# Kernel tuning notes

Measured on AMD Instinct MI355X. Metric: run time of the kernel, lower is better.

The kernel has to match this reference:

```python
import jax, jax.numpy as jnp
import numpy as np

N, E, B, EP = 100000, 1600000, 512, 200000
NIN, NEMB, HID, NL = 64, 64, 72, 3
EPS = 1e-5


def setup_inputs() -> dict:
    key = jax.random.key(0)
    ks = jax.random.split(key, 20)
    inp = {
        'x': jax.random.normal(ks[0], (N, NIN), jnp.float32),
        'emb': jax.random.normal(ks[1], (N, NEMB), jnp.float32),
        'assign': jax.random.uniform(ks[2], (N, B), jnp.float32),
        'edge_index': jax.random.randint(ks[3], (2, E), 0, N, jnp.int64),
        'pedge_index': jax.random.randint(ks[4], (2, EP), 0, B, jnp.int64),
        # params (xavier-ish scale)
        'node_w': jax.random.normal(ks[5], (NIN, HID), jnp.float32) / np.sqrt(NIN),
        'node_b': jnp.zeros((HID,), jnp.float32),
        'emb_w': jax.random.normal(ks[6], (NEMB, HID), jnp.float32) / np.sqrt(NEMB),
        'emb_b': jnp.zeros((HID,), jnp.float32),
        'conv_winit': jax.random.normal(ks[7], (NL, HID, HID), jnp.float32) / np.sqrt(HID),
        'conv_wroot': jax.random.normal(ks[8], (NL, HID, HID), jnp.float32) / np.sqrt(HID),
        'conv_bias': jnp.zeros((NL, HID), jnp.float32),
        'bn_gamma': jnp.ones((NL, HID), jnp.float32),
        'bn_beta': jnp.zeros((NL, HID), jnp.float32),
        'mlp_w1': jax.random.normal(ks[9], (12 * HID, HID), jnp.float32) / np.sqrt(12 * HID),
        'mlp_b1': jnp.zeros((HID,), jnp.float32),
        'mlp_w2': jax.random.normal(ks[10], (HID, 1), jnp.float32) / np.sqrt(HID),
        'mlp_b2': jnp.zeros((1,), jnp.float32),
    }
    return inp


def _forward(x, emb, assign, node_w, node_b, emb_w, emb_b, conv_winit,
             conv_wroot, conv_bias, bn_gamma, bn_beta, mlp_w1, mlp_b1,
             mlp_w2, mlp_b2, edge_index, pedge_index):
    n = x.shape[0]
    nb = assign.shape[1]
    row, col = edge_index[0], edge_index[1]
    # gcn_norm without self-loops (ARMAConv): D^{-1/2} A D^{-1/2}
    deg = jax.ops.segment_sum(jnp.ones((row.shape[0],), x.dtype), col, num_segments=n)
    dis = jnp.where(deg > 0, jax.lax.rsqrt(jnp.maximum(deg, 1.0)) * jnp.where(deg > 0, 1.0, 0.0), 0.0)
    dis = jnp.where(deg > 0, deg ** -0.5, 0.0)
    norm = dis[row] * dis[col]

    h = jax.nn.relu(x @ node_w + node_b)  # [N, HID]
    for l in range(NL):
        # ARMAConv K=1, T=1: relu(A_hat (h Wi) + h Wr + b)
        m = norm[:, None] * (h @ conv_winit[l])[row]        # [E, HID]
        agg = jax.ops.segment_sum(m, col, num_segments=n)   # [N, HID]
        h = jax.nn.relu(agg + h @ conv_wroot[l] + conv_bias[l])
        # F.relu applied again in forward (idempotent), then BatchNorm (training stats)
        mu = h.mean(0)
        var = ((h - mu) ** 2).mean(0)
        h = (h - mu) * jax.lax.rsqrt(var + EPS) * bn_gamma[l] + bn_beta[l]

    e = jax.nn.relu(emb @ emb_w + emb_b)
    z = jnp.concatenate([h, e], axis=-1)  # [N, 2*HID]

    batch = jnp.argmax(assign, axis=-1)
    cnt = jax.ops.segment_sum(jnp.ones((n,), z.dtype), batch, num_segments=nb)
    p1 = jax.ops.segment_sum(z, batch, num_segments=nb)
    p2 = jax.ops.segment_max(z, batch, num_segments=nb)
    p3 = p1 / jnp.maximum(cnt, 1.0)[:, None]
    xp = jnp.concatenate([p1, p2, p3], axis=-1)  # [B, 6*HID]

    pair = jnp.concatenate([xp[pedge_index[0]], xp[pedge_index[1]]], axis=1)  # [EP, 12*HID]
    out = jnp.tanh(pair @ mlp_w1 + mlp_b1) @ mlp_w2 + mlp_b2
    return out


def reference(x, emb, assign, edge_index, pedge_index, node_w, node_b, emb_w,
              emb_b, conv_winit, conv_wroot, conv_bias, bn_gamma, bn_beta,
              mlp_w1, mlp_b1, mlp_w2, mlp_b2):
    return _forward(x, emb, assign, node_w, node_b, emb_w, emb_b, conv_winit,
                    conv_wroot, conv_bias, bn_gamma, bn_beta, mlp_w1, mlp_b1,
                    mlp_w2, mlp_b2, edge_index, pedge_index)
```

## Files before the change

kernel.cpp:

```cpp
#include <hip/hip_runtime.h>
#include <hip/hip_bf16.h>

#define HID 72
#define EPSV 1e-5f
#define CAP 64

__device__ __forceinline__ float tanh_fast(float x) {
    float cx = fminf(fmaxf(x, -15.f), 15.f);
    float e = __expf(2.f * cx);
    return __fdividef(e - 1.f, e + 1.f);
}
__device__ __forceinline__ void fma4(float4& a, float w, const float4 v) {
    a.x += w * v.x; a.y += w * v.y; a.z += w * v.z; a.w += w * v.w;
}

__global__ void k_init(int* deg, float* stats, int* bcnt, int N, int statlen, int B) {
    int i = blockIdx.x * blockDim.x + threadIdx.x;
    if (i < N) deg[i] = 0;
    if (i < statlen) stats[i] = 0.f;
    if (i < B) bcnt[i] = 0;
}

__global__ __launch_bounds__(256) void k_fillcap(const int* __restrict__ row, const int* __restrict__ col,
                                                 int* __restrict__ deg, int* __restrict__ csr_r, int E) {
    int e = blockIdx.x * blockDim.x + threadIdx.x;
    if (e < E) {
        int c = col[e];
        int pos = atomicAdd(&deg[c], 1);
        if (pos < CAP) csr_r[(size_t)c * CAP + pos] = row[e];
    }
}

__global__ void k_dis(const int* __restrict__ deg, float* __restrict__ dis, int N) {
    int i = blockIdx.x * blockDim.x + threadIdx.x;
    if (i < N) {
        int d = deg[i];
        dis[i] = (d > 0) ? rsqrtf((float)d) : 0.f;
    }
}

#define DP 76
template <int K>
__global__ __launch_bounds__(256) void k_dense_t(const float* __restrict__ xin, const float* __restrict__ W,
                                                 const float* __restrict__ bias, float* __restrict__ out, int N) {
    __shared__ float hs[128][DP];
    __shared__ float ws[HID][DP];
    int tid = threadIdx.x;
    int n0 = blockIdx.x * 128;
    for (int i = tid; i < K * HID; i += 256) {
        int k = i / HID, f = i % HID;
        ws[f][k] = W[i];
    }
    for (int i = tid; i < 128 * K; i += 256) {
        int n = i / K, f = i % K;
        int gn = n0 + n;
        hs[n][f] = (gn < N) ? xin[(size_t)gn * K + f] : 0.f;
    }
    __syncthreads();
    int tn = tid & 31;
    int tf = (tid >> 5) * 9;
    float acc[4][9];
    #pragma unroll
    for (int j = 0; j < 9; j++) {
        float b = bias[tf + j];
        acc[0][j] = b; acc[1][j] = b; acc[2][j] = b; acc[3][j] = b;
    }
    #pragma unroll 2
    for (int k4 = 0; k4 < K / 4; k4++) {
        int k = k4 * 4;
        float4 h0 = *(const float4*)&hs[tn][k];
        float4 h1 = *(const float4*)&hs[tn + 32][k];
        float4 h2 = *(const float4*)&hs[tn + 64][k];
        float4 h3 = *(const float4*)&hs[tn + 96][k];
        #pragma unroll
        for (int j = 0; j < 9; j++) {
            float4 w = *(const float4*)&ws[tf + j][k];
            acc[0][j] += h0.x * w.x + h0.y * w.y + h0.z * w.z + h0.w * w.w;
            acc[1][j] += h1.x * w.x + h1.y * w.y + h1.z * w.z + h1.w * w.w;
            acc[2][j] += h2.x * w.x + h2.y * w.y + h2.z * w.z + h2.w * w.w;
            acc[3][j] += h3.x * w.x + h3.y * w.y + h3.z * w.z + h3.w * w.w;
        }
    }
    #pragma unroll
    for (int i = 0; i < 4; i++) {
        int gn = n0 + tn + 32 * i;
        if (gn >= N) continue;
        float* dst = out + (size_t)gn * HID + tf;
        #pragma unroll
        for (int j = 0; j < 9; j++) dst[j] = fmaxf(acc[i][j], 0.f);
    }
}

#define CP 76
template <bool BN>
__global__ __launch_bounds__(256) void k_conv_t(const float* t, const float* __restrict__ stats,
                                                const float* __restrict__ gamma, const float* __restrict__ beta,
                                                const float* __restrict__ wi, const float* __restrict__ wr,
                                                const float* __restrict__ cb, float* __restrict__ hw,
                                                float* agg, int N, float invN) {
    __shared__ float hs[64][CP];
    __shared__ float ws[2 * HID][CP];
    int tid = threadIdx.x;
    int n0 = blockIdx.x * 64;
    for (int i = tid; i < HID * 2 * HID; i += 256) {
        int k = i / (2 * HID), f = i % (2 * HID);
        ws[f][k] = (f < HID) ? wi[k * HID + f] : wr[k * HID + (f - HID)];
    }
    for (int i = tid; i < 64 * HID; i += 256) {
        int n = i / HID, f = i % HID;
        int gn = n0 + n;
        float v = (gn < N) ? t[(size_t)gn * HID + f] : 0.f;
        if constexpr (BN) {
            float mu = stats[f] * invN;
            float var = stats[HID + f] * invN - mu * mu;
            v = (v - mu) * rsqrtf(var + EPSV) * gamma[f] + beta[f];
        }
        hs[n][f] = v;
    }
    __syncthreads();
    int tn = tid & 15;
    int tf = (tid >> 4) * 9;
    float acc[4][9];
    #pragma unroll
    for (int j = 0; j < 9; j++) {
        float b = (tf >= HID) ? cb[tf - HID + j] : 0.f;
        acc[0][j] = b; acc[1][j] = b; acc[2][j] = b; acc[3][j] = b;
    }
    #pragma unroll 2
    for (int k4 = 0; k4 < HID / 4; k4++) {
        int k = k4 * 4;
        float4 h0 = *(const float4*)&hs[tn][k];
        float4 h1 = *(const float4*)&hs[tn + 16][k];
        float4 h2 = *(const float4*)&hs[tn + 32][k];
        float4 h3 = *(const float4*)&hs[tn + 48][k];
        #pragma unroll
        for (int j = 0; j < 9; j++) {
            float4 w = *(const float4*)&ws[tf + j][k];
            acc[0][j] += h0.x * w.x + h0.y * w.y + h0.z * w.z + h0.w * w.w;
            acc[1][j] += h1.x * w.x + h1.y * w.y + h1.z * w.z + h1.w * w.w;
            acc[2][j] += h2.x * w.x + h2.y * w.y + h2.z * w.z + h2.w * w.w;
            acc[3][j] += h3.x * w.x + h3.y * w.y + h3.z * w.z + h3.w * w.w;
        }
    }
    #pragma unroll
    for (int i = 0; i < 4; i++) {
        int gn = n0 + tn + 16 * i;
        if (gn >= N) continue;
        float* dst = (tf < HID) ? (hw + (size_t)gn * HID + tf) : (agg + (size_t)gn * HID + (tf - HID));
        #pragma unroll
        for (int j = 0; j < 9; j++) dst[j] = acc[i][j];
    }
}

__global__ __launch_bounds__(256) void k_gather9(const float* __restrict__ hw, const int* __restrict__ deg,
                                                 const int* __restrict__ csr_r, const float* __restrict__ dis,
                                                 float* t, int N) {
    int tid = blockIdx.x * blockDim.x + threadIdx.x;
    int n = tid / 9;
    int s = tid - n * 9;
    if (n >= N) return;
    float4* trow = (float4*)(t + (size_t)n * HID) + s * 2;
    float4 a0 = trow[0], a1 = trow[1];
    int d = deg[n];
    d = (d > CAP) ? CAP : d;
    float disc = dis[n];
    const int* crow = csr_r + (size_t)n * CAP;
    const float4* hb = (const float4*)hw + s * 2;
    for (int j0 = 0; j0 < d; j0 += 4) {
        int4 rr = *(const int4*)(crow + j0);
        int rem = d - j0;
        {
            float w = disc * dis[rr.x];
            const float4* hp = hb + (size_t)rr.x * 18;
            fma4(a0, w, hp[0]); fma4(a1, w, hp[1]);
        }
        if (rem > 1) {
            float w = disc * dis[rr.y];
            const float4* hp = hb + (size_t)rr.y * 18;
            fma4(a0, w, hp[0]); fma4(a1, w, hp[1]);
        }
        if (rem > 2) {
            float w = disc * dis[rr.z];
            const float4* hp = hb + (size_t)rr.z * 18;
            fma4(a0, w, hp[0]); fma4(a1, w, hp[1]);
        }
        if (rem > 3) {
            float w = disc * dis[rr.w];
            const float4* hp = hb + (size_t)rr.w * 18;
            fma4(a0, w, hp[0]); fma4(a1, w, hp[1]);
        }
    }
    trow[0] = make_float4(fmaxf(a0.x, 0.f), fmaxf(a0.y, 0.f), fmaxf(a0.z, 0.f), fmaxf(a0.w, 0.f));
    trow[1] = make_float4(fmaxf(a1.x, 0.f), fmaxf(a1.y, 0.f), fmaxf(a1.z, 0.f), fmaxf(a1.w, 0.f));
}

__global__ __launch_bounds__(256) void k_stats(const float* __restrict__ t, float* __restrict__ st, int total4) {
    __shared__ float s1[HID], s2[HID];
    int tx = threadIdx.x;
    if (tx < HID) s1[tx] = 0.f;
    else if (tx < 2 * HID) s2[tx - HID] = 0.f;
    __syncthreads();
    int stride = gridDim.x * blockDim.x;
    int i0 = blockIdx.x * blockDim.x + tx;
    int f0 = (i0 * 4) % HID;
    float a0 = 0, a1 = 0, a2 = 0, a3 = 0, q0 = 0, q1 = 0, q2 = 0, q3 = 0;
    const float4* tp = (const float4*)t;
    for (int i = i0; i < total4; i += stride) {
        float4 v = tp[i];
        a0 += v.x; q0 += v.x * v.x;
        a1 += v.y; q1 += v.y * v.y;
        a2 += v.z; q2 += v.z * v.z;
        a3 += v.w; q3 += v.w * v.w;
    }
    atomicAdd(&s1[f0 + 0], a0); atomicAdd(&s2[f0 + 0], q0);
    atomicAdd(&s1[f0 + 1], a1); atomicAdd(&s2[f0 + 1], q1);
    atomicAdd(&s1[f0 + 2], a2); atomicAdd(&s2[f0 + 2], q2);
    atomicAdd(&s1[f0 + 3], a3); atomicAdd(&s2[f0 + 3], q3);
    __syncthreads();
    if (tx < HID) {
        atomicAdd(&st[tx], s1[tx]);
        atomicAdd(&st[HID + tx], s2[tx]);
    }
}

__global__ __launch_bounds__(256) void k_argmax(const float* __restrict__ assign, int* __restrict__ batchv,
                                                int* __restrict__ bcnt, int N, int B) {
    int wib = threadIdx.x >> 6;
    int lane = threadIdx.x & 63;
    int n = blockIdx.x * (blockDim.x >> 6) + wib;
    if (n >= N) return;
    const float4* rp4 = (const float4*)(assign + (size_t)n * B);
    float best = -INFINITY;
    int bidx = 0x7fffffff;
    int nq = B / 4;
    for (int q = lane; q < nq; q += 64) {
        float4 v = rp4[q];
        int j = q * 4;
        if (v.x > best) { best = v.x; bidx = j; }
        if (v.y > best) { best = v.y; bidx = j + 1; }
        if (v.z > best) { best = v.z; bidx = j + 2; }
        if (v.w > best) { best = v.w; bidx = j + 3; }
    }
    #pragma unroll
    for (int off = 32; off > 0; off >>= 1) {
        float ov = __shfl_down(best, off);
        int oi = __shfl_down(bidx, off);
        if (ov > best || (ov == best && oi < bidx)) { best = ov; bidx = oi; }
    }
    if (lane == 0) {
        batchv[n] = bidx;
        atomicAdd(&bcnt[bidx], 1);
    }
}

__global__ __launch_bounds__(1024) void k_bscan(const int* __restrict__ bcnt, int* __restrict__ boffs,
                                                int* __restrict__ bcur, int B) {
    __shared__ int lds[1024];
    int t = threadIdx.x;
    int v = (t < B) ? bcnt[t] : 0;
    lds[t] = v;
    __syncthreads();
    for (int off = 1; off < 1024; off <<= 1) {
        int x = (t >= off) ? lds[t - off] : 0;
        __syncthreads();
        lds[t] += x;
        __syncthreads();
    }
    if (t < B) {
        int excl = lds[t] - v;
        boffs[t] = excl;
        bcur[t] = excl;
    }
}

__global__ void k_bfill(const int* __restrict__ batchv, int* __restrict__ bcur, int* __restrict__ nlist, int N) {
    int n = blockIdx.x * blockDim.x + threadIdx.x;
    if (n < N) {
        int b = batchv[n];
        int pos = atomicAdd(&bcur[b], 1);
        nlist[pos] = n;
    }
}

__global__ __launch_bounds__(576) void k_poolB(const float* __restrict__ t2, const float* __restrict__ ebuf,
                                               const float* __restrict__ stats2, const float* __restrict__ g2,
                                               const float* __restrict__ bt2, const int* __restrict__ boffs,
                                               const int* __restrict__ bcnt, const int* __restrict__ nlist,
                                               float* __restrict__ xp, float invN) {
    __shared__ float ls[4][2 * HID], lm[4][2 * HID];
    int b = blockIdx.x;
    int tid = threadIdx.x;
    int f = tid % (2 * HID);
    int ch = tid / (2 * HID);
    bool isH = f < HID;
    float a = 1.f, sh = 0.f;
    const float* src;
    if (isH) {
        float s1v = stats2[f], s2v = stats2[HID + f];
        float mu = s1v * invN;
        float var = s2v * invN - mu * mu;
        float inv = rsqrtf(var + EPSV);
        a = inv * g2[f];
        sh = bt2[f] - mu * a;
        src = t2 + f;
    } else {
        src = ebuf + (f - HID);
    }
    int s = boffs[b];
    int c = bcnt[b];
    int e = s + c;
    float sum = 0.f, mx = -INFINITY;
    for (int i = s + ch; i < e; i += 4) {
        float v = src[(size_t)nlist[i] * HID] * a + sh;
        sum += v;
        mx = fmaxf(mx, v);
    }
    ls[ch][f] = sum;
    lm[ch][f] = mx;
    __syncthreads();
    if (ch == 0) {
        float stot = ls[0][f] + ls[1][f] + ls[2][f] + ls[3][f];
        float mtot = fmaxf(fmaxf(lm[0][f], lm[1][f]), fmaxf(lm[2][f], lm[3][f]));
        float* xr = xp + (size_t)b * (6 * HID);
        xr[f] = stot;
        xr[2 * HID + f] = mtot;
        xr[4 * HID + f] = stot / fmaxf((float)c, 1.f);
    }
}

__global__ __launch_bounds__(192) void k_uv(const float* __restrict__ xp, const float* __restrict__ w1,
                                            const float* __restrict__ b1, float* __restrict__ U,
                                            float* __restrict__ V) {
    int b = blockIdx.x;
    int t = threadIdx.x;
    if (t >= 2 * HID) return;
    int half = t / HID;
    int f = t % HID;
    const float* xr = xp + (size_t)b * (6 * HID);
    const float* wb = w1 + (size_t)half * (6 * HID) * HID + f;
    float acc = (half == 0) ? b1[f] : 0.f;
    #pragma unroll 4
    for (int k = 0; k < 6 * HID; k++) acc += xr[k] * wb[(size_t)k * HID];
    if (half == 0) U[(size_t)b * HID + f] = acc;
    else           V[(size_t)b * HID + f] = acc;
}

__global__ __launch_bounds__(256) void k_edge(const int* __restrict__ pe, const float* __restrict__ U,
                                              const float* __restrict__ V, const float* __restrict__ w2,
                                              const float* __restrict__ b2, float* __restrict__ out, int EP) {
    int ep = blockIdx.x * blockDim.x + threadIdx.x;
    if (ep >= EP) return;
    int a = pe[ep];
    int b = pe[EP + ep];
    const float4* up = (const float4*)(U + (size_t)a * HID);
    const float4* vp = (const float4*)(V + (size_t)b * HID);
    float s = 0.f;
    #pragma unroll
    for (int q = 0; q < HID / 4; q++) {
        float4 u = up[q];
        float4 v = vp[q];
        s += tanh_fast(u.x + v.x) * w2[q * 4 + 0];
        s += tanh_fast(u.y + v.y) * w2[q * 4 + 1];
        s += tanh_fast(u.z + v.z) * w2[q * 4 + 2];
        s += tanh_fast(u.w + v.w) * w2[q * 4 + 3];
    }
    out[ep] = s + b2[0];
}

extern "C" void kernel_launch(void* const* d_in, const int* in_sizes, int n_in,
                              void* d_out, int out_size, void* d_ws, size_t ws_size,
                              hipStream_t stream) {
    const float* x       = (const float*)d_in[0];
    const float* emb     = (const float*)d_in[1];
    const float* assign  = (const float*)d_in[2];
    const int*   ei      = (const int*)d_in[3];
    const int*   pe      = (const int*)d_in[4];
    const float* node_w  = (const float*)d_in[5];
    const float* node_b  = (const float*)d_in[6];
    const float* emb_w   = (const float*)d_in[7];
    const float* emb_b   = (const float*)d_in[8];
    const float* conv_wi = (const float*)d_in[9];
    const float* conv_wr = (const float*)d_in[10];
    const float* conv_b  = (const float*)d_in[11];
    const float* bn_g    = (const float*)d_in[12];
    const float* bn_b    = (const float*)d_in[13];
    const float* w1      = (const float*)d_in[14];
    const float* b1      = (const float*)d_in[15];
    const float* w2      = (const float*)d_in[16];
    const float* b2      = (const float*)d_in[17];

    int N = in_sizes[0] / 64;
    int B = in_sizes[2] / N;
    int E = in_sizes[3] / 2;
    int EP = in_sizes[4] / 2;
    float invN = 1.0f / (float)N;

    char* wp = (char*)d_ws;
    auto alloc = [&](size_t nbytes) -> void* {
        void* p = (void*)wp;
        wp += (nbytes + 255) & ~(size_t)255;
        return p;
    };
    float* t_buf  = (float*)alloc((size_t)N * HID * 4);
    float* hw     = (float*)alloc((size_t)N * HID * 4);
    float* e_buf  = (float*)alloc((size_t)N * HID * 4);
    int*   csr_r  = (int*)alloc((size_t)N * CAP * 4);
    int*   deg    = (int*)alloc((size_t)N * 4);
    float* dis    = (float*)alloc((size_t)N * 4);
    int*   batchv = (int*)alloc((size_t)N * 4);
    int*   nlist  = (int*)alloc((size_t)N * 4);
    float* stats  = (float*)alloc((size_t)3 * 2 * HID * 4);
    int*   bcnt   = (int*)alloc((size_t)B * 4);
    int*   boffs  = (int*)alloc((size_t)B * 4);
    int*   bcur   = (int*)alloc((size_t)B * 4);
    float* xp     = (float*)alloc((size_t)B * 6 * HID * 4);
    float* Ub     = (float*)alloc((size_t)B * HID * 4);
    float* Vb     = (float*)alloc((size_t)B * HID * 4);

    const int* row = ei;
    const int* col = ei + E;

    int nb256_N = (N + 255) / 256;
    int nb256_E = (E + 255) / 256;

    k_init<<<nb256_N, 256, 0, stream>>>(deg, stats, bcnt, N, 3 * 2 * HID, B);
    k_fillcap<<<nb256_E, 256, 0, stream>>>(row, col, deg, csr_r, E);
    k_dis<<<nb256_N, 256, 0, stream>>>(deg, dis, N);

    k_dense_t<64><<<(N + 127) / 128, 256, 0, stream>>>(x, node_w, node_b, t_buf, N);
    k_dense_t<64><<<(N + 127) / 128, 256, 0, stream>>>(emb, emb_w, emb_b, e_buf, N);

    for (int l = 0; l < 3; l++) {
        const float* wi = conv_wi + (size_t)l * HID * HID;
        const float* wr = conv_wr + (size_t)l * HID * HID;
        const float* cb = conv_b + (size_t)l * HID;
        if (l == 0)
            k_conv_t<false><<<(N + 63) / 64, 256, 0, stream>>>(t_buf, nullptr, nullptr, nullptr,
                                                               wi, wr, cb, hw, t_buf, N, invN);
        else
            k_conv_t<true><<<(N + 63) / 64, 256, 0, stream>>>(t_buf, stats + (size_t)(l - 1) * 2 * HID,
                                                              bn_g + (size_t)(l - 1) * HID,
                                                              bn_b + (size_t)(l - 1) * HID,
                                                              wi, wr, cb, hw, t_buf, N, invN);
        k_gather9<<<(9 * N + 255) / 256, 256, 0, stream>>>(hw, deg, csr_r, dis, t_buf, N);
        k_stats<<<288, 256, 0, stream>>>(t_buf, stats + (size_t)l * 2 * HID, N * HID / 4);
    }

    k_argmax<<<(N + 3) / 4, 256, 0, stream>>>(assign, batchv, bcnt, N, B);
    k_bscan<<<1, 1024, 0, stream>>>(bcnt, boffs, bcur, B);
    k_bfill<<<nb256_N, 256, 0, stream>>>(batchv, bcur, nlist, N);
    k_poolB<<<B, 576, 0, stream>>>(t_buf, e_buf, stats + (size_t)2 * 2 * HID,
                                   bn_g + (size_t)2 * HID, bn_b + (size_t)2 * HID,
                                   boffs, bcnt, nlist, xp, invN);
    k_uv<<<B, 192, 0, stream>>>(xp, w1, b1, Ub, Vb);
    k_edge<<<(EP + 255) / 256, 256, 0, stream>>>(pe, Ub, Vb, w2, b2, (float*)d_out, EP);
}
```

Measured before the change: 1.322 ms.

## Aggregate-then-transform in bf16 with bucketed CSR construction and fused conv

Each conv layer now gathers raw neighbor features before the matrix multiply, using A(hW) = (Ah)W. Features are read from a bf16 copy, and batch-norm is folded in afterwards through a per-node sum of weighted degrees. The root and init matmuls are fused into one K=144 GEMM that also applies bias and ReLU. The CSR build changes from global atomics on a scattered array to a two-pass bucket sort that uses shared-memory atomics. Risks are bf16 precision loss in the aggregation and silently dropped edges if a bucket overflows BCAPE.

```diff
diff --git a/kernel.cpp b/kernel.cpp
--- a/kernel.cpp
+++ b/kernel.cpp
@@ -4,31 +4,90 @@
 #define HID 72
 #define EPSV 1e-5f
 #define CAP 64
+#define BCAPE 24576
+#define MAXBK 128
+
+typedef unsigned int uint;
+typedef unsigned short ushort;
 
 __device__ __forceinline__ float tanh_fast(float x) {
     float cx = fminf(fmaxf(x, -15.f), 15.f);
     float e = __expf(2.f * cx);
     return __fdividef(e - 1.f, e + 1.f);
 }
-__device__ __forceinline__ void fma4(float4& a, float w, const float4 v) {
-    a.x += w * v.x; a.y += w * v.y; a.z += w * v.z; a.w += w * v.w;
-}
-
-__global__ void k_init(int* deg, float* stats, int* bcnt, int N, int statlen, int B) {
-    int i = blockIdx.x * blockDim.x + threadIdx.x;
-    if (i < N) deg[i] = 0;
-    if (i < statlen) stats[i] = 0.f;
-    if (i < B) bcnt[i] = 0;
-}
-
-__global__ __launch_bounds__(256) void k_fillcap(const int* __restrict__ row, const int* __restrict__ col,
-                                                 int* __restrict__ deg, int* __restrict__ csr_r, int E) {
-    int e = blockIdx.x * blockDim.x + threadIdx.x;
-    if (e < E) {
-        int c = col[e];
-        int pos = atomicAdd(&deg[c], 1);
-        if (pos < CAP) csr_r[(size_t)c * CAP + pos] = row[e];
-    }
+__device__ __forceinline__ ushort to_bf16(float f) {
+    uint u = __float_as_uint(f);
+    uint r = (u + 0x7FFFu + ((u >> 16) & 1u)) >> 16;
+    return (ushort)r;
+}
+__device__ __forceinline__ void bf2x(uint u, float& lo, float& hi) {
+    lo = __uint_as_float(u << 16);
+    hi = __uint_as_float(u & 0xFFFF0000u);
+}
+
+__global__ __launch_bounds__(1024) void k_init(float* stats, int* bcnt, int* gbk, int B) {
+    int t = threadIdx.x;
+    if (t < 3 * 2 * HID) stats[t] = 0.f;
+    if (t < B) bcnt[t] = 0;
+    if (t < MAXBK) gbk[t] = 0;
+}
+
+__global__ __launch_bounds__(1024) void k_bktA(const int* __restrict__ row, const int* __restrict__ col,
+                                               int2* __restrict__ ebkt, int* __restrict__ gbk, int E) {
+    __shared__ int cnt[MAXBK], gpos[MAXBK], cur[MAXBK];
+    int tid = threadIdx.x;
+    if (tid < MAXBK) cnt[tid] = 0;
+    __syncthreads();
+    int base = blockIdx.x * 4096;
+    int r[4], c[4], b[4];
+    bool v[4];
+    #pragma unroll
+    for (int j = 0; j < 4; j++) {
+        int e = base + j * 1024 + tid;
+        v[j] = e < E;
+        if (v[j]) {
+            r[j] = row[e];
+            c[j] = col[e];
+            b[j] = c[j] >> 10;
+            atomicAdd(&cnt[b[j]], 1);
+        }
+    }
+    __syncthreads();
+    if (tid < MAXBK) {
+        cur[tid] = 0;
+        if (cnt[tid] > 0) gpos[tid] = atomicAdd(&gbk[tid], cnt[tid]);
+    }
+    __syncthreads();
+    #pragma unroll
+    for (int j = 0; j < 4; j++) {
+        if (v[j]) {
+            int slot = atomicAdd(&cur[b[j]], 1);
+            int dst = gpos[b[j]] + slot;
+            if (dst < BCAPE) ebkt[(size_t)b[j] * BCAPE + dst] = make_int2(r[j], c[j]);
+        }
+    }
+}
+
+__global__ __launch_bounds__(1024) void k_bktB(const int2* __restrict__ ebkt, const int* __restrict__ gbk,
+                                               int* __restrict__ deg, int* __restrict__ csr_r, int N) {
+    __shared__ int ldeg[1024];
+    int b = blockIdx.x;
+    int tid = threadIdx.x;
+    ldeg[tid] = 0;
+    __syncthreads();
+    int cnt = gbk[b];
+    cnt = (cnt > BCAPE) ? BCAPE : cnt;
+    int nbase = b << 10;
+    const int2* src = ebkt + (size_t)b * BCAPE;
+    for (int i = tid; i < cnt; i += 1024) {
+        int2 e = src[i];
+        int lc = e.y - nbase;
+        int pos = atomicAdd(&ldeg[lc], 1);
+        if (pos < CAP) csr_r[(size_t)e.y * CAP + pos] = e.x;
+    }
+    __syncthreads();
+    int gn = nbase + tid;
+    if (gn < N) deg[gn] = ldeg[tid];
 }
 
 __global__ void k_dis(const int* __restrict__ deg, float* __restrict__ dis, int N) {
@@ -40,9 +99,10 @@
 }
 
 #define DP 76
-template <int K>
+template <int K, bool WBF>
 __global__ __launch_bounds__(256) void k_dense_t(const float* __restrict__ xin, const float* __restrict__ W,
-                                                 const float* __restrict__ bias, float* __restrict__ out, int N) {
+                                                 const float* __restrict__ bias, float* __restrict__ out,
+                                                 ushort* __restrict__ out_bf, int N) {
     __shared__ float hs[128][DP];
     __shared__ float ws[HID][DP];
     int tid = threadIdx.x;
@@ -87,111 +147,123 @@
         if (gn >= N) continue;
         float* dst = out + (size_t)gn * HID + tf;
         #pragma unroll
-        for (int j = 0; j < 9; j++) dst[j] = fmaxf(acc[i][j], 0.f);
-    }
-}
-
-#define CP 76
-template <bool BN>
-__global__ __launch_bounds__(256) void k_conv_t(const float* t, const float* __restrict__ stats,
-                                                const float* __restrict__ gamma, const float* __restrict__ beta,
-                                                const float* __restrict__ wi, const float* __restrict__ wr,
-                                                const float* __restrict__ cb, float* __restrict__ hw,
-                                                float* agg, int N, float invN) {
-    __shared__ float hs[64][CP];
-    __shared__ float ws[2 * HID][CP];
-    int tid = threadIdx.x;
-    int n0 = blockIdx.x * 64;
-    for (int i = tid; i < HID * 2 * HID; i += 256) {
-        int k = i / (2 * HID), f = i % (2 * HID);
-        ws[f][k] = (f < HID) ? wi[k * HID + f] : wr[k * HID + (f - HID)];
-    }
-    for (int i = tid; i < 64 * HID; i += 256) {
-        int n = i / HID, f = i % HID;
-        int gn = n0 + n;
-        float v = (gn < N) ? t[(size_t)gn * HID + f] : 0.f;
-        if constexpr (BN) {
-            float mu = stats[f] * invN;
-            float var = stats[HID + f] * invN - mu * mu;
-            v = (v - mu) * rsqrtf(var + EPSV) * gamma[f] + beta[f];
-        }
-        hs[n][f] = v;
-    }
-    __syncthreads();
-    int tn = tid & 15;
-    int tf = (tid >> 4) * 9;
-    float acc[4][9];
-    #pragma unroll
-    for (int j = 0; j < 9; j++) {
-        float b = (tf >= HID) ? cb[tf - HID + j] : 0.f;
-        acc[0][j] = b; acc[1][j] = b; acc[2][j] = b; acc[3][j] = b;
-    }
-    #pragma unroll 2
-    for (int k4 = 0; k4 < HID / 4; k4++) {
-        int k = k4 * 4;
-        float4 h0 = *(const float4*)&hs[tn][k];
-        float4 h1 = *(const float4*)&hs[tn + 16][k];
-        float4 h2 = *(const float4*)&hs[tn + 32][k];
-        float4 h3 = *(const float4*)&hs[tn + 48][k];
-        #pragma unroll
         for (int j = 0; j < 9; j++) {
-            float4 w = *(const float4*)&ws[tf + j][k];
-            acc[0][j] += h0.x * w.x + h0.y * w.y + h0.z * w.z + h0.w * w.w;
-            acc[1][j] += h1.x * w.x + h1.y * w.y + h1.z * w.z + h1.w * w.w;
-            acc[2][j] += h2.x * w.x + h2.y * w.y + h2.z * w.z + h2.w * w.w;
-            acc[3][j] += h3.x * w.x + h3.y * w.y + h3.z * w.z + h3.w * w.w;
-        }
-    }
-    #pragma unroll
-    for (int i = 0; i < 4; i++) {
-        int gn = n0 + tn + 16 * i;
-        if (gn >= N) continue;
-        float* dst = (tf < HID) ? (hw + (size_t)gn * HID + tf) : (agg + (size_t)gn * HID + (tf - HID));
-        #pragma unroll
-        for (int j = 0; j < 9; j++) dst[j] = acc[i][j];
-    }
-}
-
-__global__ __launch_bounds__(256) void k_gather9(const float* __restrict__ hw, const int* __restrict__ deg,
+            float v = fmaxf(acc[i][j], 0.f);
+            dst[j] = v;
+            if constexpr (WBF) out_bf[(size_t)gn * HID + tf + j] = to_bf16(v);
+        }
+    }
+}
+
+__global__ __launch_bounds__(256) void k_gather9(const ushort* __restrict__ t_bf, const int* __restrict__ deg,
                                                  const int* __restrict__ csr_r, const float* __restrict__ dis,
-                                                 float* t, int N) {
+                                                 float* __restrict__ ah, float* __restrict__ wsum, int N) {
     int tid = blockIdx.x * blockDim.x + threadIdx.x;
     int n = tid / 9;
     int s = tid - n * 9;
     if (n >= N) return;
-    float4* trow = (float4*)(t + (size_t)n * HID) + s * 2;
-    float4 a0 = trow[0], a1 = trow[1];
+    float4 a0 = make_float4(0.f, 0.f, 0.f, 0.f);
+    float4 a1 = make_float4(0.f, 0.f, 0.f, 0.f);
+    float sd = 0.f;
     int d = deg[n];
     d = (d > CAP) ? CAP : d;
     float disc = dis[n];
     const int* crow = csr_r + (size_t)n * CAP;
-    const float4* hb = (const float4*)hw + s * 2;
     for (int j0 = 0; j0 < d; j0 += 4) {
         int4 rr = *(const int4*)(crow + j0);
         int rem = d - j0;
-        {
-            float w = disc * dis[rr.x];
-            const float4* hp = hb + (size_t)rr.x * 18;
-            fma4(a0, w, hp[0]); fma4(a1, w, hp[1]);
-        }
-        if (rem > 1) {
-            float w = disc * dis[rr.y];
-            const float4* hp = hb + (size_t)rr.y * 18;
-            fma4(a0, w, hp[0]); fma4(a1, w, hp[1]);
-        }
-        if (rem > 2) {
-            float w = disc * dis[rr.z];
-            const float4* hp = hb + (size_t)rr.z * 18;
-            fma4(a0, w, hp[0]); fma4(a1, w, hp[1]);
-        }
-        if (rem > 3) {
-            float w = disc * dis[rr.w];
-            const float4* hp = hb + (size_t)rr.w * 18;
-            fma4(a0, w, hp[0]); fma4(a1, w, hp[1]);
-        }
-    }
-    trow[0] = make_float4(fmaxf(a0.x, 0.f), fmaxf(a0.y, 0.f), fmaxf(a0.z, 0.f), fmaxf(a0.w, 0.f));
-    trow[1] = make_float4(fmaxf(a1.x, 0.f), fmaxf(a1.y, 0.f), fmaxf(a1.z, 0.f), fmaxf(a1.w, 0.f));
+        #pragma unroll
+        for (int q = 0; q < 4; q++) {
+            if (q < rem) {
+                int r = (q == 0) ? rr.x : (q == 1) ? rr.y : (q == 2) ? rr.z : rr.w;
+                float dr = dis[r];
+                float w = disc * dr;
+                sd += dr;
+                uint4 p = *(const uint4*)(t_bf + (size_t)r * HID + s * 8);
+                float f0, f1, f2, f3, f4, f5, f6, f7;
+                bf2x(p.x, f0, f1); bf2x(p.y, f2, f3);
+                bf2x(p.z, f4, f5); bf2x(p.w, f6, f7);
+                a0.x += w * f0; a0.y += w * f1; a0.z += w * f2; a0.w += w * f3;
+                a1.x += w * f4; a1.y += w * f5; a1.z += w * f6; a1.w += w * f7;
+            }
+        }
+    }
+    float4* op = (float4*)(ah + (size_t)n * HID + s * 8);
+    op[0] = a0;
+    op[1] = a1;
+    if (s == 0) wsum[n] = disc * sd;
+}
+
+#define KP 148
+template <bool BN>
+__global__ __launch_bounds__(256) void k_conv_f(float* t, const float* __restrict__ ah,
+                                                const float* __restrict__ wsum, const float* __restrict__ stats,
+                                                const float* __restrict__ gamma, const float* __restrict__ beta,
+                                                const float* __restrict__ wi, const float* __restrict__ wr,
+                                                const float* __restrict__ cb, ushort* __restrict__ t_bf,
+                                                int N, float invN, int write_bf) {
+    __shared__ float ks[32][KP];
+    __shared__ float ws[HID][KP];
+    __shared__ float asl[HID], shl[HID];
+    int tid = threadIdx.x;
+    int n0 = blockIdx.x * 32;
+    if constexpr (BN) {
+        if (tid < HID) {
+            float mu = stats[tid] * invN;
+            float var = stats[HID + tid] * invN - mu * mu;
+            float a = rsqrtf(var + EPSV) * gamma[tid];
+            asl[tid] = a;
+            shl[tid] = beta[tid] - mu * a;
+        }
+        __syncthreads();
+    }
+    for (int i = tid; i < HID * 2 * HID; i += 256) {
+        int k = i / HID, f = i % HID;
+        ws[f][k] = (k < HID) ? wi[k * HID + f] : wr[(k - HID) * HID + f];
+    }
+    for (int i = tid; i < 32 * 2 * HID; i += 256) {
+        int n = i / (2 * HID), k = i % (2 * HID);
+        int gn = n0 + n;
+        float v = 0.f;
+        if (gn < N) {
+            if (k < HID) {
+                v = ah[(size_t)gn * HID + k];
+                if constexpr (BN) v = asl[k] * v + wsum[gn] * shl[k];
+            } else {
+                int f = k - HID;
+                v = t[(size_t)gn * HID + f];
+                if constexpr (BN) v = asl[f] * v + shl[f];
+            }
+        }
+        ks[n][k] = v;
+    }
+    __syncthreads();
+    int tn = tid & 31;
+    int tf = (tid >> 5) * 9;
+    float acc[9];
+    #pragma unroll
+    for (int j = 0; j < 9; j++) acc[j] = cb[tf + j];
+    #pragma unroll 2
+    for (int k4 = 0; k4 < 2 * HID / 4; k4++) {
+        int k = k4 * 4;
+        float4 h = *(const float4*)&ks[tn][k];
+        #pragma unroll
+        for (int j = 0; j < 9; j++) {
+            float4 w = *(const float4*)&ws[tf + j][k];
+            acc[j] += h.x * w.x + h.y * w.y + h.z * w.z + h.w * w.w;
+        }
+    }
+    int gn = n0 + tn;
+    if (gn < N) {
+        float* dst = t + (size_t)gn * HID + tf;
+        ushort* db = t_bf + (size_t)gn * HID + tf;
+        #pragma unroll
+        for (int j = 0; j < 9; j++) {
+            float v = fmaxf(acc[j], 0.f);
+            dst[j] = v;
+            if (write_bf) db[j] = to_bf16(v);
+        }
+    }
 }
 
 __global__ __launch_bounds__(256) void k_stats(const float* __restrict__ t, float* __restrict__ st, int total4) {
@@ -394,6 +466,7 @@
     int E = in_sizes[3] / 2;
     int EP = in_sizes[4] / 2;
     float invN = 1.0f / (float)N;
+    int BK = (N + 1023) >> 10;
 
     char* wp = (char*)d_ws;
     auto alloc = [&](size_t nbytes) -> void* {
@@ -401,48 +474,53 @@
         wp += (nbytes + 255) & ~(size_t)255;
         return p;
     };
-    float* t_buf  = (float*)alloc((size_t)N * HID * 4);
-    float* hw     = (float*)alloc((size_t)N * HID * 4);
-    float* e_buf  = (float*)alloc((size_t)N * HID * 4);
-    int*   csr_r  = (int*)alloc((size_t)N * CAP * 4);
-    int*   deg    = (int*)alloc((size_t)N * 4);
-    float* dis    = (float*)alloc((size_t)N * 4);
-    int*   batchv = (int*)alloc((size_t)N * 4);
-    int*   nlist  = (int*)alloc((size_t)N * 4);
-    float* stats  = (float*)alloc((size_t)3 * 2 * HID * 4);
-    int*   bcnt   = (int*)alloc((size_t)B * 4);
-    int*   boffs  = (int*)alloc((size_t)B * 4);
-    int*   bcur   = (int*)alloc((size_t)B * 4);
-    float* xp     = (float*)alloc((size_t)B * 6 * HID * 4);
-    float* Ub     = (float*)alloc((size_t)B * HID * 4);
-    float* Vb     = (float*)alloc((size_t)B * HID * 4);
+    float*  t_buf  = (float*)alloc((size_t)N * HID * 4);
+    ushort* t_bf   = (ushort*)alloc((size_t)N * HID * 2);
+    float*  e_buf  = (float*)alloc((size_t)N * HID * 4);
+    float*  ah     = (float*)alloc((size_t)N * HID * 4);
+    float*  wsum   = (float*)alloc((size_t)N * 4);
+    int2*   ebkt   = (int2*)alloc((size_t)MAXBK * BCAPE * 8);
+    int*    gbk    = (int*)alloc((size_t)MAXBK * 4);
+    int*    csr_r  = (int*)alloc((size_t)N * CAP * 4);
+    int*    deg    = (int*)alloc((size_t)N * 4);
+    float*  dis    = (float*)alloc((size_t)N * 4);
+    int*    batchv = (int*)alloc((size_t)N * 4);
+    int*    nlist  = (int*)alloc((size_t)N * 4);
+    float*  stats  = (float*)alloc((size_t)3 * 2 * HID * 4);
+    int*    bcnt   = (int*)alloc((size_t)B * 4);
+    int*    boffs  = (int*)alloc((size_t)B * 4);
+    int*    bcur   = (int*)alloc((size_t)B * 4);
+    float*  xp     = (float*)alloc((size_t)B * 6 * HID * 4);
+    float*  Ub     = (float*)alloc((size_t)B * HID * 4);
+    float*  Vb     = (float*)alloc((size_t)B * HID * 4);
 
     const int* row = ei;
     const int* col = ei + E;
-
     int nb256_N = (N + 255) / 256;
-    int nb256_E = (E + 255) / 256;
-
-    k_init<<<nb256_N, 256, 0, stream>>>(deg, stats, bcnt, N, 3 * 2 * HID, B);
-    k_fillcap<<<nb256_E, 256, 0, stream>>>(row, col, deg, csr_r, E);
+
+    k_init<<<1, 1024, 0, stream>>>(stats, bcnt, gbk, B);
+    k_bktA<<<(E + 4095) / 4096, 1024, 0, stream>>>(row, col, ebkt, gbk, E);
+    k_bktB<<<BK, 1024, 0, stream>>>(ebkt, gbk, deg, csr_r, N);
     k_dis<<<nb256_N, 256, 0, stream>>>(deg, dis, N);
 
-    k_dense_t<64><<<(N + 127) / 128, 256, 0, stream>>>(x, node_w, node_b, t_buf, N);
-    k_dense_t<64><<<(N + 127) / 128, 256, 0, stream>>>(emb, emb_w, emb_b, e_buf, N);
+    k_dense_t<64, true><<<(N + 127) / 128, 256, 0, stream>>>(x, node_w, node_b, t_buf, t_bf, N);
+    k_dense_t<64, false><<<(N + 127) / 128, 256, 0, stream>>>(emb, emb_w, emb_b, e_buf, nullptr, N);
 
     for (int l = 0; l < 3; l++) {
         const float* wi = conv_wi + (size_t)l * HID * HID;
         const float* wr = conv_wr + (size_t)l * HID * HID;
         const float* cb = conv_b + (size_t)l * HID;
+        int wbf = (l < 2) ? 1 : 0;
+        k_gather9<<<(9 * N + 255) / 256, 256, 0, stream>>>(t_bf, deg, csr_r, dis, ah, wsum, N);
         if (l == 0)
-            k_conv_t<false><<<(N + 63) / 64, 256, 0, stream>>>(t_buf, nullptr, nullptr, nullptr,
-                                                               wi, wr, cb, hw, t_buf, N, invN);
+            k_conv_f<false><<<(N + 31) / 32, 256, 0, stream>>>(t_buf, ah, wsum, nullptr, nullptr, nullptr,
+                                                               wi, wr, cb, t_bf, N, invN, wbf);
         else
-            k_conv_t<true><<<(N + 63) / 64, 256, 0, stream>>>(t_buf, stats + (size_t)(l - 1) * 2 * HID,
+            k_conv_f<true><<<(N + 31) / 32, 256, 0, stream>>>(t_buf, ah, wsum,
+                                                              stats + (size_t)(l - 1) * 2 * HID,
                                                               bn_g + (size_t)(l - 1) * HID,
                                                               bn_b + (size_t)(l - 1) * HID,
-                                                              wi, wr, cb, hw, t_buf, N, invN);
-        k_gather9<<<(9 * N + 255) / 256, 256, 0, stream>>>(hw, deg, csr_r, dis, t_buf, N);
+                                                              wi, wr, cb, t_bf, N, invN, wbf);
         k_stats<<<288, 256, 0, stream>>>(t_buf, stats + (size_t)l * 2 * HID, N * HID / 4);
     }
 
```

After: 1.366 ms. 3.3% more time.
